# Performance work log

Measured on AMD Instinct MI355X. Metric: run time of the kernel, lower is better.

Reference implementation:

```python
import jax, jax.numpy as jnp
import numpy as np

N = 100000
E = 1600000
IN_C, HID_C, OUT_C = 64, 64, 40

def setup_inputs() -> dict:
    key = jax.random.key(0)
    ks = jax.random.split(key, 12)
    x = jax.random.normal(ks[0], (N, IN_C), dtype=jnp.float32)
    edge_index = jax.random.randint(ks[1], (2, E), 0, N, dtype=jnp.int32)
    def glorot(k, fan_in, fan_out):
        lim = float(np.sqrt(6.0 / (fan_in + fan_out)))
        return jax.random.uniform(k, (fan_in, fan_out), jnp.float32, -lim, lim)
    return {
        "x": x,
        "edge_index": edge_index,
        "W0_0": glorot(ks[2], IN_C, HID_C), "W1_0": glorot(ks[3], IN_C, HID_C), "b_0": jnp.zeros((HID_C,), jnp.float32),
        "W0_1": glorot(ks[4], HID_C, HID_C), "W1_1": glorot(ks[5], HID_C, HID_C), "b_1": jnp.zeros((HID_C,), jnp.float32),
        "W0_2": glorot(ks[6], HID_C, OUT_C), "W1_2": glorot(ks[7], HID_C, OUT_C), "b_2": jnp.zeros((OUT_C,), jnp.float32),
    }

def _cheb_norm(edge_index, num_nodes, dtype):
    # PyG ChebConv.__norm__ with normalization=None, edge_weight=None -> ones.
    # L = D - A; lambda_max = 2 * max(L weights); scaled: 2L/lambda_max - I.
    src, dst = edge_index[0], edge_index[1]
    w = jnp.ones((edge_index.shape[1],), dtype)
    deg = jax.ops.segment_sum(w, src, num_segments=num_nodes)
    lam = 2.0 * jnp.maximum(jnp.max(deg), jnp.max(-w))
    scale = 2.0 / lam
    norm_edge = -w * scale            # off-diagonal entries
    norm_loop = deg * scale - 1.0     # diagonal entries (self-loop mask subtracts 1)
    return norm_edge, norm_loop

def _spmm(x, src, dst, norm_edge, norm_loop, num_nodes):
    # y[i] = sum_{e: src->i} norm_e * x[src_e] + norm_loop[i] * x[i]
    msg = norm_edge[:, None] * x[src]
    return jax.ops.segment_sum(msg, dst, num_segments=num_nodes) + norm_loop[:, None] * x

def reference(x, edge_index, W0_0, W1_0, b_0, W0_1, W1_1, b_1, W0_2, W1_2, b_2):
    num_nodes = x.shape[0]
    src, dst = edge_index[0], edge_index[1]
    norm_edge, norm_loop = _cheb_norm(edge_index, num_nodes, x.dtype)

    def cheb(h, W0, W1, b):
        # K=2: out = T0(L) h W0 + T1(L) h W1 + b, T0 = I, T1 = scaled L
        Tx1 = _spmm(h, src, dst, norm_edge, norm_loop, num_nodes)
        return h @ W0 + Tx1 @ W1 + b

    h = jax.nn.relu(cheb(x, W0_0, W1_0, b_0))   # dropout is identity in eval mode
    h = jax.nn.relu(cheb(h, W0_1, W1_1, b_1))
    h = cheb(h, W0_2, W1_2, b_2)
    return jax.nn.log_softmax(h, axis=-1)
```

## Files before the change

kernel.cpp:

```cpp
#include <hip/hip_runtime.h>
#include <math.h>

#define N_NODES 100000
#define N_EDGES 1600000
#define OUTC 40
#define PAIRS40 20

#define NC 32
#define CHUNK (N_EDGES / NC)

#define RANGE_H 32768
#define NR_H 4
#define NPAD_H (NR_H * RANGE_H)

#define RANGE_F 16384
#define NR_F 7

#define SCAN_BLOCK 1024
#define SCAN_NBLK ((N_NODES + SCAN_BLOCK - 1) / SCAN_BLOCK)

typedef float vf2 __attribute__((ext_vector_type(2)));
typedef __fp16 f16x2 __attribute__((ext_vector_type(2)));

__device__ inline unsigned pack_bf16x2(float lo, float hi) {
    unsigned a = __float_as_uint(lo), b = __float_as_uint(hi);
    a = (a + 0x7fffu + ((a >> 16) & 1u)) >> 16;
    b = (b + 0x7fffu + ((b >> 16) & 1u)) & 0xffff0000u;
    return a | b;
}
__device__ inline float bf_lo(unsigned u) { return __uint_as_float(u << 16); }
__device__ inline float bf_hi(unsigned u) { return __uint_as_float(u & 0xffff0000u); }

__device__ inline unsigned pk16(float a, float b) {
    f16x2 h = __builtin_amdgcn_cvt_pkrtz(a, b);
    return __builtin_bit_cast(unsigned, h);
}
__device__ inline f16x2 uph(unsigned u) { return __builtin_bit_cast(f16x2, u); }

__device__ inline float fdot2(f16x2 a, f16x2 b, float c) {
#if __has_builtin(__builtin_amdgcn_fdot2)
    return __builtin_amdgcn_fdot2(a, b, c, false);
#else
    float d;
    asm volatile("v_dot2_f32_f16 %0, %1, %2, %3" : "=v"(d) : "v"(a), "v"(b), "v"(c));
    return d;
#endif
}

__global__ __launch_bounds__(1024) void k_hist(const int* __restrict__ src,
                                               const int* __restrict__ dst,
                                               int* __restrict__ Hs,
                                               int* __restrict__ Hd) {
    __shared__ unsigned h32[RANGE_H / 2];
    int c = blockIdx.x, r = blockIdx.y;
    const int* a = blockIdx.z ? dst : src;
    int* H = blockIdx.z ? Hd : Hs;
    for (int k = threadIdx.x; k < RANGE_H / 2; k += 1024) h32[k] = 0;
    __syncthreads();
    int r0 = r * RANGE_H;
    int e0 = c * CHUNK, e1 = e0 + CHUNK;
    for (int e = e0 + threadIdx.x; e < e1; e += 1024) {
        unsigned d = (unsigned)(a[e] - r0);
        if (d < RANGE_H) atomicAdd(&h32[d >> 1], 1u << ((d & 1) * 16));
    }
    __syncthreads();
    for (int k = threadIdx.x; k < RANGE_H; k += 1024)
        H[c * NPAD_H + r0 + k] = (int)((h32[k >> 1] >> ((k & 1) * 16)) & 0xffffu);
}

__global__ __launch_bounds__(SCAN_BLOCK) void k_scan1(const int* __restrict__ Hs,
                                                      const int* __restrict__ Hd,
                                                      int* __restrict__ rowptr,
                                                      int* __restrict__ blocksum,
                                                      int* __restrict__ deg_src,
                                                      int* __restrict__ maxdeg) {
    __shared__ int buf[2][SCAN_BLOCK];
    int t = threadIdx.x;
    int i = blockIdx.x * SCAN_BLOCK + t;
    int vs = 0, vd = 0;
    if (i < N_NODES) {
        #pragma unroll
        for (int c = 0; c < NC; c++) { vs += Hs[c * NPAD_H + i]; vd += Hd[c * NPAD_H + i]; }
        deg_src[i] = vs;
    }
    int m = vs;
    for (int off = 32; off; off >>= 1) m = max(m, __shfl_down(m, off));
    if ((t & 63) == 0) atomicMax(maxdeg, m);
    int pd = (vd + 7) & ~7;
    int cur = 0;
    buf[0][t] = pd;
    __syncthreads();
    for (int off = 1; off < SCAN_BLOCK; off <<= 1) {
        int nv = buf[cur][t];
        if (t >= off) nv += buf[cur][t - off];
        buf[1 - cur][t] = nv;
        cur = 1 - cur;
        __syncthreads();
    }
    int incl = buf[cur][t];
    if (i < N_NODES) rowptr[i + 1] = incl;
    if (t == SCAN_BLOCK - 1) blocksum[blockIdx.x] = incl;
}

__global__ __launch_bounds__(SCAN_BLOCK) void k_finalize(const int* __restrict__ blocksum,
                                                         int* __restrict__ rowptr,
                                                         int* __restrict__ Hd,
                                                         int* __restrict__ csr_src) {
    __shared__ int soff;
    int t = threadIdx.x, blk = blockIdx.x;
    if (t == 0) {
        int r = 0;
        for (int j = 0; j < blk; j++) r += blocksum[j];
        soff = r;
        if (blk == 0) rowptr[0] = 0;
    }
    __syncthreads();
    int i = blk * SCAN_BLOCK + t;
    if (i >= N_NODES) return;
    int tmp[NC];
    int s = 0;
    #pragma unroll
    for (int c = 0; c < NC; c++) { tmp[c] = Hd[c * NPAD_H + i]; s += tmp[c]; }
    int rf = rowptr[i + 1] + soff;
    rowptr[i + 1] = rf;
    int pd = (s + 7) & ~7;
    int run = rf - pd;
    #pragma unroll
    for (int c = 0; c < NC; c++) { Hd[c * NPAD_H + i] = run; run += tmp[c]; }
    for (int k = run; k < rf; k++) csr_src[k] = N_NODES;
}

__global__ __launch_bounds__(1024) void k_fill2(const int* __restrict__ src,
                                                const int* __restrict__ dst,
                                                const int* __restrict__ basepos,
                                                int* __restrict__ csr_src) {
    __shared__ int pos[RANGE_F];
    int c = blockIdx.x, r = blockIdx.y;
    int r0 = r * RANGE_F;
    for (int k = threadIdx.x; k < RANGE_F; k += 1024) pos[k] = basepos[c * NPAD_H + r0 + k];
    __syncthreads();
    int e0 = c * CHUNK, e1 = e0 + CHUNK;
    for (int e = e0 + threadIdx.x; e < e1; e += 1024) {
        unsigned d = (unsigned)(dst[e] - r0);
        if (d < RANGE_F) {
            int s = src[e];
            int p = atomicAdd(&pos[d], 1);
            csr_src[p] = s;
        }
    }
}

__global__ __launch_bounds__(256, 8) void k_gemm64(const float* __restrict__ hf,
                                                   const float* __restrict__ W0,
                                                   const float* __restrict__ W1,
                                                   const float* __restrict__ b,
                                                   const int* __restrict__ deg_src,
                                                   const int* __restrict__ maxdeg,
                                                   unsigned* __restrict__ G0b,
                                                   unsigned short* __restrict__ G1f8) {
    __shared__ uint4 swu[32 * 32];
    __shared__ unsigned shu[32 * 32];
    int t = threadIdx.x;
    const float2* W02 = (const float2*)W0;
    const float2* W12 = (const float2*)W1;
    for (int cell = t; cell < 1024; cell += 256) {
        int kp = cell >> 5, c2 = cell & 31;
        float2 a  = W02[(kp * 2) * 32 + c2];
        float2 bb = W02[(kp * 2 + 1) * 32 + c2];
        float2 cc = W12[(kp * 2) * 32 + c2];
        float2 dd = W12[(kp * 2 + 1) * 32 + c2];
        swu[cell] = make_uint4(pk16(a.x, bb.x), pk16(a.y, bb.y), pk16(cc.x, dd.x), pk16(cc.y, dd.y));
    }
    int i0 = blockIdx.x * 32;
    const float4* h4 = (const float4*)(hf + (size_t)i0 * 64);
    {
        float4 f0 = h4[t * 2], f1 = h4[t * 2 + 1];
        ((uint4*)shu)[t] = make_uint4(pk16(f0.x, f0.y), pk16(f0.z, f0.w), pk16(f1.x, f1.y), pk16(f1.z, f1.w));
    }
    if (blockIdx.x == 0 && t < 16) ((unsigned*)G1f8)[N_NODES * 16 + t] = 0;
    __syncthreads();
    int c2 = t & 31, rg = t >> 5;
    float scale = 1.0f / (float)(*maxdeg);
    float2 b2 = ((const float2*)b)[c2];
    float a0x[4], a0y[4], a1x[4], a1y[4];
    #pragma unroll
    for (int p = 0; p < 4; p++) { a0x[p] = b2.x; a0y[p] = b2.y; a1x[p] = 0.f; a1y[p] = 0.f; }
    #pragma unroll 8
    for (int kp = 0; kp < 32; kp++) {
        uint4 w = swu[kp * 32 + c2];
        f16x2 w0x = uph(w.x), w0y = uph(w.y), w1x = uph(w.z), w1y = uph(w.w);
        #pragma unroll
        for (int p = 0; p < 4; p++) {
            f16x2 h2 = uph(shu[(rg + 8 * p) * 32 + kp]);
            a0x[p] = fdot2(h2, w0x, a0x[p]);
            a0y[p] = fdot2(h2, w0y, a0y[p]);
            a1x[p] = fdot2(h2, w1x, a1x[p]);
            a1y[p] = fdot2(h2, w1y, a1y[p]);
        }
    }
    #pragma unroll
    for (int p = 0; p < 4; p++) {
        int row = i0 + rg + 8 * p;
        float nl = (float)deg_src[row] * scale - 1.0f;
        G0b[row * 32 + c2] = pack_bf16x2(a0x[p] + nl * a1x[p], a0y[p] + nl * a1y[p]);
        int pk = __builtin_amdgcn_cvt_pk_fp8_f32(a1x[p], a1y[p], 0, false);
        G1f8[row * 32 + c2] = (unsigned short)(pk & 0xffff);
    }
}

__global__ __launch_bounds__(256, 6) void k_fs64_g64(const unsigned* __restrict__ G0b_in,
                                                     const unsigned char* __restrict__ g1_in,
                                                     const int* __restrict__ rowptr,
                                                     const int* __restrict__ csr_src,
                                                     const int* __restrict__ deg_src,
                                                     const int* __restrict__ maxdeg,
                                                     const float* __restrict__ W0,
                                                     const float* __restrict__ W1,
                                                     const float* __restrict__ b,
                                                     unsigned* __restrict__ G0b_out,
                                                     unsigned short* __restrict__ G1f8_out) {
    __shared__ uint4 swu[32 * 32];
    __shared__ unsigned shu[32 * 32];
    int t = threadIdx.x;
    const float2* W02 = (const float2*)W0;
    const float2* W12 = (const float2*)W1;
    for (int cell = t; cell < 1024; cell += 256) {
        int kp = cell >> 5, c2 = cell & 31;
        float2 a  = W02[(kp * 2) * 32 + c2];
        float2 bb = W02[(kp * 2 + 1) * 32 + c2];
        float2 cc = W12[(kp * 2) * 32 + c2];
        float2 dd = W12[(kp * 2 + 1) * 32 + c2];
        swu[cell] = make_uint4(pk16(a.x, bb.x), pk16(a.y, bb.y), pk16(cc.x, dd.x), pk16(cc.y, dd.y));
    }
    int waveId = t >> 6, lane = t & 63;
    int ch = lane & 7;
    int local = waveId * 8 + (lane >> 3);
    int node = blockIdx.x * 32 + local;
    float scale = 1.0f / (float)(*maxdeg);
    int e0 = rowptr[node], e1 = rowptr[node + 1];
    int octbase = lane & 56;
    vf2 acc[4];
    acc[0] = 0.f; acc[1] = 0.f; acc[2] = 0.f; acc[3] = 0.f;
    uint2 u[8];
    int idxB = 0;
    int e = e0;
    if (e < e1) {
        int idxA = csr_src[e + ch];
        if (e + 8 < e1) idxB = csr_src[e + 8 + ch];
        #pragma unroll
        for (int j = 0; j < 8; j++) {
            int s = __shfl(idxA, octbase | j);
            u[j] = ((const uint2*)(g1_in + (size_t)s * 64))[ch];
        }
    }
    while (e < e1) {
        int en = e + 8;
        int idxC = 0;
        if (en + 8 < e1) idxC = csr_src[en + 8 + ch];
        uint2 n[8];
        if (en < e1) {
            #pragma unroll
            for (int j = 0; j < 8; j++) {
                int s = __shfl(idxB, octbase | j);
                n[j] = ((const uint2*)(g1_in + (size_t)s * 64))[ch];
            }
        }
        #pragma unroll
        for (int j = 0; j < 8; j++) {
            acc[0] += __builtin_amdgcn_cvt_pk_f32_fp8((int)u[j].x, false);
            acc[1] += __builtin_amdgcn_cvt_pk_f32_fp8((int)u[j].x, true);
            acc[2] += __builtin_amdgcn_cvt_pk_f32_fp8((int)u[j].y, false);
            acc[3] += __builtin_amdgcn_cvt_pk_f32_fp8((int)u[j].y, true);
        }
        #pragma unroll
        for (int j = 0; j < 8; j++) u[j] = n[j];
        idxB = idxC;
        e = en;
    }
    uint4 g = ((const uint4*)(G0b_in + (size_t)node * 32))[ch];
    float v0 = fmaxf(bf_lo(g.x) - scale * acc[0].x, 0.f);
    float v1 = fmaxf(bf_hi(g.x) - scale * acc[0].y, 0.f);
    float v2 = fmaxf(bf_lo(g.y) - scale * acc[1].x, 0.f);
    float v3 = fmaxf(bf_hi(g.y) - scale * acc[1].y, 0.f);
    float v4 = fmaxf(bf_lo(g.z) - scale * acc[2].x, 0.f);
    float v5 = fmaxf(bf_hi(g.z) - scale * acc[2].y, 0.f);
    float v6 = fmaxf(bf_lo(g.w) - scale * acc[3].x, 0.f);
    float v7 = fmaxf(bf_hi(g.w) - scale * acc[3].y, 0.f);
    ((uint4*)shu)[local * 8 + ch] = make_uint4(pk16(v0, v1), pk16(v2, v3), pk16(v4, v5), pk16(v6, v7));
    if (blockIdx.x == 0 && t < 16) ((unsigned*)G1f8_out)[N_NODES * 16 + t] = 0;
    __syncthreads();
    int c2 = t & 31, rg = t >> 5;
    int i0 = blockIdx.x * 32;
    float2 b2 = ((const float2*)b)[c2];
    float a0x[4], a0y[4], a1x[4], a1y[4];
    #pragma unroll
    for (int p = 0; p < 4; p++) { a0x[p] = b2.x; a0y[p] = b2.y; a1x[p] = 0.f; a1y[p] = 0.f; }
    #pragma unroll 8
    for (int kp = 0; kp < 32; kp++) {
        uint4 w = swu[kp * 32 + c2];
        f16x2 w0x = uph(w.x), w0y = uph(w.y), w1x = uph(w.z), w1y = uph(w.w);
        #pragma unroll
        for (int p = 0; p < 4; p++) {
            f16x2 h2 = uph(shu[(rg + 8 * p) * 32 + kp]);
            a0x[p] = fdot2(h2, w0x, a0x[p]);
            a0y[p] = fdot2(h2, w0y, a0y[p]);
            a1x[p] = fdot2(h2, w1x, a1x[p]);
            a1y[p] = fdot2(h2, w1y, a1y[p]);
        }
    }
    #pragma unroll
    for (int p = 0; p < 4; p++) {
        int row = i0 + rg + 8 * p;
        float nl = (float)deg_src[row] * scale - 1.0f;
        G0b_out[row * 32 + c2] = pack_bf16x2(a0x[p] + nl * a1x[p], a0y[p] + nl * a1y[p]);
        int pk = __builtin_amdgcn_cvt_pk_fp8_f32(a1x[p], a1y[p], 0, false);
        G1f8_out[row * 32 + c2] = (unsigned short)(pk & 0xffff);
    }
}

__global__ __launch_bounds__(256, 6) void k_fs64_g40(const unsigned* __restrict__ G0b_in,
                                                     const unsigned char* __restrict__ g1_in,
                                                     const int* __restrict__ rowptr,
                                                     const int* __restrict__ csr_src,
                                                     const int* __restrict__ deg_src,
                                                     const int* __restrict__ maxdeg,
                                                     const float* __restrict__ W0,
                                                     const float* __restrict__ W1,
                                                     const float* __restrict__ b,
                                                     unsigned* __restrict__ G0b_out,
                                                     unsigned short* __restrict__ G1f8_out) {
    __shared__ uint4 swu[32 * PAIRS40];
    __shared__ unsigned shu[32 * 32];
    int t = threadIdx.x;
    const float2* W02 = (const float2*)W0;
    const float2* W12 = (const float2*)W1;
    for (int cell = t; cell < 32 * PAIRS40; cell += 256) {
        int kp = cell / PAIRS40, c2 = cell % PAIRS40;
        float2 a  = W02[(kp * 2) * PAIRS40 + c2];
        float2 bb = W02[(kp * 2 + 1) * PAIRS40 + c2];
        float2 cc = W12[(kp * 2) * PAIRS40 + c2];
        float2 dd = W12[(kp * 2 + 1) * PAIRS40 + c2];
        swu[cell] = make_uint4(pk16(a.x, bb.x), pk16(a.y, bb.y), pk16(cc.x, dd.x), pk16(cc.y, dd.y));
    }
    int waveId = t >> 6, lane = t & 63;
    int ch = lane & 7;
    int local = waveId * 8 + (lane >> 3);
    int node = blockIdx.x * 32 + local;
    float scale = 1.0f / (float)(*maxdeg);
    int e0 = rowptr[node], e1 = rowptr[node + 1];
    int octbase = lane & 56;
    vf2 acc[4];
    acc[0] = 0.f; acc[1] = 0.f; acc[2] = 0.f; acc[3] = 0.f;
    uint2 u[8];
    int idxB = 0;
    int e = e0;
    if (e < e1) {
        int idxA = csr_src[e + ch];
        if (e + 8 < e1) idxB = csr_src[e + 8 + ch];
        #pragma unroll
        for (int j = 0; j < 8; j++) {
            int s = __shfl(idxA, octbase | j);
            u[j] = ((const uint2*)(g1_in + (size_t)s * 64))[ch];
        }
    }
    while (e < e1) {
        int en = e + 8;
        int idxC = 0;
        if (en + 8 < e1) idxC = csr_src[en + 8 + ch];
        uint2 n[8];
        if (en < e1) {
            #pragma unroll
            for (int j = 0; j < 8; j++) {
                int s = __shfl(idxB, octbase | j);
                n[j] = ((const uint2*)(g1_in + (size_t)s * 64))[ch];
            }
        }
        #pragma unroll
        for (int j = 0; j < 8; j++) {
            acc[0] += __builtin_amdgcn_cvt_pk_f32_fp8((int)u[j].x, false);
            acc[1] += __builtin_amdgcn_cvt_pk_f32_fp8((int)u[j].x, true);
            acc[2] += __builtin_amdgcn_cvt_pk_f32_fp8((int)u[j].y, false);
            acc[3] += __builtin_amdgcn_cvt_pk_f32_fp8((int)u[j].y, true);
        }
        #pragma unroll
        for (int j = 0; j < 8; j++) u[j] = n[j];
        idxB = idxC;
        e = en;
    }
    uint4 g = ((const uint4*)(G0b_in + (size_t)node * 32))[ch];
    float v0 = fmaxf(bf_lo(g.x) - scale * acc[0].x, 0.f);
    float v1 = fmaxf(bf_hi(g.x) - scale * acc[0].y, 0.f);
    float v2 = fmaxf(bf_lo(g.y) - scale * acc[1].x, 0.f);
    float v3 = fmaxf(bf_hi(g.y) - scale * acc[1].y, 0.f);
    float v4 = fmaxf(bf_lo(g.z) - scale * acc[2].x, 0.f);
    float v5 = fmaxf(bf_hi(g.z) - scale * acc[2].y, 0.f);
    float v6 = fmaxf(bf_lo(g.w) - scale * acc[3].x, 0.f);
    float v7 = fmaxf(bf_hi(g.w) - scale * acc[3].y, 0.f);
    ((uint4*)shu)[local * 8 + ch] = make_uint4(pk16(v0, v1), pk16(v2, v3), pk16(v4, v5), pk16(v6, v7));
    if (blockIdx.x == 0 && t < 10) ((unsigned*)G1f8_out)[N_NODES * 10 + t] = 0;
    __syncthreads();
    int c2 = t & 31, rg = t >> 5;
    if (c2 >= PAIRS40) return;
    int i0 = blockIdx.x * 32;
    float2 b2 = ((const float2*)b)[c2];
    float a0x[4], a0y[4], a1x[4], a1y[4];
    #pragma unroll
    for (int p = 0; p < 4; p++) { a0x[p] = b2.x; a0y[p] = b2.y; a1x[p] = 0.f; a1y[p] = 0.f; }
    #pragma unroll 8
    for (int kp = 0; kp < 32; kp++) {
        uint4 w = swu[kp * PAIRS40 + c2];
        f16x2 w0x = uph(w.x), w0y = uph(w.y), w1x = uph(w.z), w1y = uph(w.w);
        #pragma unroll
        for (int p = 0; p < 4; p++) {
            f16x2 h2 = uph(shu[(rg + 8 * p) * 32 + kp]);
            a0x[p] = fdot2(h2, w0x, a0x[p]);
            a0y[p] = fdot2(h2, w0y, a0y[p]);
            a1x[p] = fdot2(h2, w1x, a1x[p]);
            a1y[p] = fdot2(h2, w1y, a1y[p]);
        }
    }
    #pragma unroll
    for (int p = 0; p < 4; p++) {
        int row = i0 + rg + 8 * p;
        float nl = (float)deg_src[row] * scale - 1.0f;
        G0b_out[row * PAIRS40 + c2] = pack_bf16x2(a0x[p] + nl * a1x[p], a0y[p] + nl * a1y[p]);
        int pk = __builtin_amdgcn_cvt_pk_fp8_f32(a1x[p], a1y[p], 0, false);
        G1f8_out[row * PAIRS40 + c2] = (unsigned short)(pk & 0xffff);
    }
}

__global__ __launch_bounds__(256, 6) void k_spmm40(const unsigned* __restrict__ G0b,
                                                   const unsigned char* __restrict__ g1,
                                                   const int* __restrict__ rowptr,
                                                   const int* __restrict__ csr_src,
                                                   const int* __restrict__ maxdeg,
                                                   float* __restrict__ out) {
    int t = threadIdx.x;
    int waveId = t >> 6, lane = t & 63;
    int ch = lane & 7;
    bool act = ch < 5;
    int node = blockIdx.x * 32 + waveId * 8 + (lane >> 3);
    float scale = 1.0f / (float)(*maxdeg);
    int e0 = rowptr[node], e1 = rowptr[node + 1];
    int octbase = lane & 56;
    vf2 acc[4];
    acc[0] = 0.f; acc[1] = 0.f; acc[2] = 0.f; acc[3] = 0.f;
    uint2 u[8];
    int idxB = 0;
    int e = e0;
    if (e < e1) {
        int idxA = csr_src[e + ch];
        if (e + 8 < e1) idxB = csr_src[e + 8 + ch];
        #pragma unroll
        for (int j = 0; j < 8; j++) {
            int s = __shfl(idxA, octbase | j);
            if (act) u[j] = ((const uint2*)(g1 + (size_t)s * 40))[ch];
        }
    }
    while (e < e1) {
        int en = e + 8;
        int idxC = 0;
        if (en + 8 < e1) idxC = csr_src[en + 8 + ch];
        uint2 n[8];
        if (en < e1) {
            #pragma unroll
            for (int j = 0; j < 8; j++) {
                int s = __shfl(idxB, octbase | j);
                if (act) n[j] = ((const uint2*)(g1 + (size_t)s * 40))[ch];
            }
        }
        if (act) {
            #pragma unroll
            for (int j = 0; j < 8; j++) {
                acc[0] += __builtin_amdgcn_cvt_pk_f32_fp8((int)u[j].x, false);
                acc[1] += __builtin_amdgcn_cvt_pk_f32_fp8((int)u[j].x, true);
                acc[2] += __builtin_amdgcn_cvt_pk_f32_fp8((int)u[j].y, false);
                acc[3] += __builtin_amdgcn_cvt_pk_f32_fp8((int)u[j].y, true);
            }
        }
        #pragma unroll
        for (int j = 0; j < 8; j++) u[j] = n[j];
        idxB = idxC;
        e = en;
    }
    float v[8];
    float m = -INFINITY;
    if (act) {
        uint4 g = ((const uint4*)(G0b + (size_t)node * PAIRS40))[ch];
        v[0] = bf_lo(g.x) - scale * acc[0].x;
        v[1] = bf_hi(g.x) - scale * acc[0].y;
        v[2] = bf_lo(g.y) - scale * acc[1].x;
        v[3] = bf_hi(g.y) - scale * acc[1].y;
        v[4] = bf_lo(g.z) - scale * acc[2].x;
        v[5] = bf_hi(g.z) - scale * acc[2].y;
        v[6] = bf_lo(g.w) - scale * acc[3].x;
        v[7] = bf_hi(g.w) - scale * acc[3].y;
        #pragma unroll
        for (int q = 0; q < 8; q++) m = fmaxf(m, v[q]);
    }
    m = fmaxf(m, __shfl_xor(m, 1));
    m = fmaxf(m, __shfl_xor(m, 2));
    m = fmaxf(m, __shfl_xor(m, 4));
    float s = 0.f;
    if (act) {
        #pragma unroll
        for (int q = 0; q < 8; q++) s += __expf(v[q] - m);
    }
    s += __shfl_xor(s, 1);
    s += __shfl_xor(s, 2);
    s += __shfl_xor(s, 4);
    float ls = __logf(s);
    if (act) {
        float4 oA, oB;
        oA.x = v[0] - m - ls; oA.y = v[1] - m - ls; oA.z = v[2] - m - ls; oA.w = v[3] - m - ls;
        oB.x = v[4] - m - ls; oB.y = v[5] - m - ls; oB.z = v[6] - m - ls; oB.w = v[7] - m - ls;
        float4* o4 = (float4*)(out + (size_t)node * 40);
        o4[ch * 2] = oA;
        o4[ch * 2 + 1] = oB;
    }
}


extern "C" void kernel_launch(void* const* d_in, const int* in_sizes, int n_in,
                              void* d_out, int out_size, void* d_ws, size_t ws_size,
                              hipStream_t stream) {
    const float* x   = (const float*)d_in[0];
    const int* ei    = (const int*)d_in[1];
    const int* src   = ei;
    const int* dst   = ei + N_EDGES;
    const float* W0_0 = (const float*)d_in[2];
    const float* W1_0 = (const float*)d_in[3];
    const float* b_0  = (const float*)d_in[4];
    const float* W0_1 = (const float*)d_in[5];
    const float* W1_1 = (const float*)d_in[6];
    const float* b_1  = (const float*)d_in[7];
    const float* W0_2 = (const float*)d_in[8];
    const float* W1_2 = (const float*)d_in[9];
    const float* b_2  = (const float*)d_in[10];
    float* outp = (float*)d_out;

    int* ip = (int*)d_ws;
    int* deg_src  = ip;
    int* rowptr   = ip + 100000;
    int* blocksum = ip + 200064;
    int* maxdeg   = ip + 200192;
    int* csr_src  = ip + 200256;
    int* Hs       = ip + 2700256;
    int* Hd       = ip + 6894560;
    unsigned* GA0 = (unsigned*)(ip + 11088864);
    unsigned short* GA1 = (unsigned short*)(ip + 14288864);
    unsigned* GB0 = (unsigned*)(ip + 15888928);
    unsigned short* GB1 = (unsigned short*)(ip + 19088928);

    (void)hipMemsetAsync(maxdeg, 0, sizeof(int), stream);

    k_hist<<<dim3(NC, NR_H, 2), 1024, 0, stream>>>(src, dst, Hs, Hd);
    k_scan1<<<SCAN_NBLK, SCAN_BLOCK, 0, stream>>>(Hs, Hd, rowptr, blocksum, deg_src, maxdeg);
    k_finalize<<<SCAN_NBLK, SCAN_BLOCK, 0, stream>>>(blocksum, rowptr, Hd, csr_src);
    k_fill2<<<dim3(NC, NR_F), 1024, 0, stream>>>(src, dst, Hd, csr_src);

    const int GS = N_NODES / 32;

    k_gemm64<<<GS, 256, 0, stream>>>(x, W0_0, W1_0, b_0, deg_src, maxdeg, GA0, GA1);
    k_fs64_g64<<<GS, 256, 0, stream>>>(GA0, (const unsigned char*)GA1, rowptr, csr_src,
                                       deg_src, maxdeg, W0_1, W1_1, b_1, GB0, GB1);
    k_fs64_g40<<<GS, 256, 0, stream>>>(GB0, (const unsigned char*)GB1, rowptr, csr_src,
                                       deg_src, maxdeg, W0_2, W1_2, b_2, GA0, GA1);
    k_spmm40<<<GS, 256, 0, stream>>>(GA0, (const unsigned char*)GA1, rowptr, csr_src, maxdeg, outp);
}
```

Measured before the change: 296.2 us.

## Replace chunked LDS histogram CSR build with global atomic degree count and fill

Replaces the per-chunk shared-memory histograms (32 chunks by node ranges, with large Hs/Hd workspaces) with direct global atomicAdd degree counting and an atomic-position scatter fill. This removes the 32-way strided reads and writes over big histogram buffers in the scan and finalize steps and shrinks the workspace. In exchange it relies on contended global atomics over random node indices, and the order of entries within each CSR row becomes nondeterministic.

```diff
diff --git a/kernel.cpp b/kernel.cpp
--- a/kernel.cpp
+++ b/kernel.cpp
@@ -5,16 +5,6 @@
 #define N_EDGES 1600000
 #define OUTC 40
 #define PAIRS40 20
-
-#define NC 32
-#define CHUNK (N_EDGES / NC)
-
-#define RANGE_H 32768
-#define NR_H 4
-#define NPAD_H (NR_H * RANGE_H)
-
-#define RANGE_F 16384
-#define NR_F 7
 
 #define SCAN_BLOCK 1024
 #define SCAN_NBLK ((N_NODES + SCAN_BLOCK - 1) / SCAN_BLOCK)
@@ -47,42 +37,27 @@
 #endif
 }
 
-__global__ __launch_bounds__(1024) void k_hist(const int* __restrict__ src,
-                                               const int* __restrict__ dst,
-                                               int* __restrict__ Hs,
-                                               int* __restrict__ Hd) {
-    __shared__ unsigned h32[RANGE_H / 2];
-    int c = blockIdx.x, r = blockIdx.y;
-    const int* a = blockIdx.z ? dst : src;
-    int* H = blockIdx.z ? Hd : Hs;
-    for (int k = threadIdx.x; k < RANGE_H / 2; k += 1024) h32[k] = 0;
-    __syncthreads();
-    int r0 = r * RANGE_H;
-    int e0 = c * CHUNK, e1 = e0 + CHUNK;
-    for (int e = e0 + threadIdx.x; e < e1; e += 1024) {
-        unsigned d = (unsigned)(a[e] - r0);
-        if (d < RANGE_H) atomicAdd(&h32[d >> 1], 1u << ((d & 1) * 16));
-    }
-    __syncthreads();
-    for (int k = threadIdx.x; k < RANGE_H; k += 1024)
-        H[c * NPAD_H + r0 + k] = (int)((h32[k >> 1] >> ((k & 1) * 16)) & 0xffffu);
-}
-
-__global__ __launch_bounds__(SCAN_BLOCK) void k_scan1(const int* __restrict__ Hs,
-                                                      const int* __restrict__ Hd,
+__global__ __launch_bounds__(256) void k_deg(const int* __restrict__ src,
+                                             const int* __restrict__ dst,
+                                             int* __restrict__ deg_src,
+                                             int* __restrict__ deg_dst) {
+    int i = blockIdx.x * 256 + threadIdx.x;
+    if (i < N_EDGES) {
+        atomicAdd(&deg_src[src[i]], 1);
+        atomicAdd(&deg_dst[dst[i]], 1);
+    }
+}
+
+__global__ __launch_bounds__(SCAN_BLOCK) void k_scan1(const int* __restrict__ deg_src,
+                                                      const int* __restrict__ deg_dst,
                                                       int* __restrict__ rowptr,
                                                       int* __restrict__ blocksum,
-                                                      int* __restrict__ deg_src,
                                                       int* __restrict__ maxdeg) {
     __shared__ int buf[2][SCAN_BLOCK];
     int t = threadIdx.x;
     int i = blockIdx.x * SCAN_BLOCK + t;
     int vs = 0, vd = 0;
-    if (i < N_NODES) {
-        #pragma unroll
-        for (int c = 0; c < NC; c++) { vs += Hs[c * NPAD_H + i]; vd += Hd[c * NPAD_H + i]; }
-        deg_src[i] = vs;
-    }
+    if (i < N_NODES) { vs = deg_src[i]; vd = deg_dst[i]; }
     int m = vs;
     for (int off = 32; off; off >>= 1) m = max(m, __shfl_down(m, off));
     if ((t & 63) == 0) atomicMax(maxdeg, m);
@@ -103,8 +78,9 @@
 }
 
 __global__ __launch_bounds__(SCAN_BLOCK) void k_finalize(const int* __restrict__ blocksum,
+                                                         const int* __restrict__ deg_dst,
                                                          int* __restrict__ rowptr,
-                                                         int* __restrict__ Hd,
+                                                         int* __restrict__ pos,
                                                          int* __restrict__ csr_src) {
     __shared__ int soff;
     int t = threadIdx.x, blk = blockIdx.x;
@@ -117,36 +93,23 @@
     __syncthreads();
     int i = blk * SCAN_BLOCK + t;
     if (i >= N_NODES) return;
-    int tmp[NC];
-    int s = 0;
-    #pragma unroll
-    for (int c = 0; c < NC; c++) { tmp[c] = Hd[c * NPAD_H + i]; s += tmp[c]; }
+    int vd = deg_dst[i];
+    int pd = (vd + 7) & ~7;
     int rf = rowptr[i + 1] + soff;
     rowptr[i + 1] = rf;
-    int pd = (s + 7) & ~7;
-    int run = rf - pd;
-    #pragma unroll
-    for (int c = 0; c < NC; c++) { Hd[c * NPAD_H + i] = run; run += tmp[c]; }
-    for (int k = run; k < rf; k++) csr_src[k] = N_NODES;
-}
-
-__global__ __launch_bounds__(1024) void k_fill2(const int* __restrict__ src,
-                                                const int* __restrict__ dst,
-                                                const int* __restrict__ basepos,
-                                                int* __restrict__ csr_src) {
-    __shared__ int pos[RANGE_F];
-    int c = blockIdx.x, r = blockIdx.y;
-    int r0 = r * RANGE_F;
-    for (int k = threadIdx.x; k < RANGE_F; k += 1024) pos[k] = basepos[c * NPAD_H + r0 + k];
-    __syncthreads();
-    int e0 = c * CHUNK, e1 = e0 + CHUNK;
-    for (int e = e0 + threadIdx.x; e < e1; e += 1024) {
-        unsigned d = (unsigned)(dst[e] - r0);
-        if (d < RANGE_F) {
-            int s = src[e];
-            int p = atomicAdd(&pos[d], 1);
-            csr_src[p] = s;
-        }
+    int base = rf - pd;
+    pos[i] = base;
+    for (int k = base + vd; k < rf; k++) csr_src[k] = N_NODES;
+}
+
+__global__ __launch_bounds__(256) void k_fill(const int* __restrict__ src,
+                                              const int* __restrict__ dst,
+                                              int* __restrict__ pos,
+                                              int* __restrict__ csr_src) {
+    int i = blockIdx.x * 256 + threadIdx.x;
+    if (i < N_EDGES) {
+        int p = atomicAdd(&pos[dst[i]], 1);
+        csr_src[p] = src[i];
     }
 }
 
@@ -541,23 +504,24 @@
 
     int* ip = (int*)d_ws;
     int* deg_src  = ip;
-    int* rowptr   = ip + 100000;
-    int* blocksum = ip + 200064;
-    int* maxdeg   = ip + 200192;
-    int* csr_src  = ip + 200256;
-    int* Hs       = ip + 2700256;
-    int* Hd       = ip + 6894560;
-    unsigned* GA0 = (unsigned*)(ip + 11088864);
-    unsigned short* GA1 = (unsigned short*)(ip + 14288864);
-    unsigned* GB0 = (unsigned*)(ip + 15888928);
-    unsigned short* GB1 = (unsigned short*)(ip + 19088928);
-
-    (void)hipMemsetAsync(maxdeg, 0, sizeof(int), stream);
-
-    k_hist<<<dim3(NC, NR_H, 2), 1024, 0, stream>>>(src, dst, Hs, Hd);
-    k_scan1<<<SCAN_NBLK, SCAN_BLOCK, 0, stream>>>(Hs, Hd, rowptr, blocksum, deg_src, maxdeg);
-    k_finalize<<<SCAN_NBLK, SCAN_BLOCK, 0, stream>>>(blocksum, rowptr, Hd, csr_src);
-    k_fill2<<<dim3(NC, NR_F), 1024, 0, stream>>>(src, dst, Hd, csr_src);
+    int* deg_dst  = ip + 100032;
+    int* maxdeg   = ip + 200064;
+    int* rowptr   = ip + 200128;
+    int* blocksum = ip + 300192;
+    int* pos      = ip + 300320;
+    int* csr_src  = ip + 400352;
+    unsigned* GA0 = (unsigned*)(ip + 2900352);
+    unsigned short* GA1 = (unsigned short*)(ip + 6100352);
+    unsigned* GB0 = (unsigned*)(ip + 7700368);
+    unsigned short* GB1 = (unsigned short*)(ip + 10900368);
+
+    (void)hipMemsetAsync(ip, 0, 200128 * sizeof(int), stream);
+
+    const int EB = (N_EDGES + 255) / 256;
+    k_deg<<<EB, 256, 0, stream>>>(src, dst, deg_src, deg_dst);
+    k_scan1<<<SCAN_NBLK, SCAN_BLOCK, 0, stream>>>(deg_src, deg_dst, rowptr, blocksum, maxdeg);
+    k_finalize<<<SCAN_NBLK, SCAN_BLOCK, 0, stream>>>(blocksum, deg_dst, rowptr, pos, csr_src);
+    k_fill<<<EB, 256, 0, stream>>>(src, dst, pos, csr_src);
 
     const int GS = N_NODES / 32;
 
```

New measurement: 480.1 us. 62.1% more time.
